# Performance work log

Hardware: AMD Instinct MI355X
Metric: run time of the kernel (lower is better)

The kernel has to match this reference:

```python
import jax, jax.numpy as jnp
import numpy as np

N, D, E, H, K = 16384, 1024, 16, 4096, 2


def setup_inputs() -> dict:
    key = jax.random.key(0)
    ks = jax.random.split(key, 6)
    s = 0.02
    return {
        "x": jax.random.normal(ks[0], (N, D), jnp.float32),
        "Wr": jax.random.normal(ks[1], (D, E), jnp.float32) * s,
        "br": jnp.zeros((E,), jnp.float32),
        "Wn": jax.random.normal(ks[2], (D, E), jnp.float32) * s,
        "bn": jnp.zeros((E,), jnp.float32),
        "W1": jax.random.normal(ks[3], (E, D, H), jnp.float32) * s,
        "b1": jnp.zeros((E, H), jnp.float32),
        "W2": jax.random.normal(ks[4], (E, H, 1), jnp.float32) * s,
        "b2": jnp.zeros((E, 1), jnp.float32),
        "k": K,
    }


def reference(x, Wr, br, Wn, bn, W1, b1, W2, b2, k):
    # Router. NOTE: faithful to source — top-k and scattered values come from
    # noise_logits; logits/noise feed only noisy_logits which is dead (only used
    # as a shape template for the -inf tensor), so the randn noise is omitted.
    noise_logits = x @ Wn + bn                      # [N, E]
    vals, idx = jax.lax.top_k(noise_logits, k)      # [N, k]
    # softmax over sparse(-inf filled) logits == softmax over top-k values,
    # scattered back; non-selected experts get exactly 0.
    probs = jax.nn.softmax(vals, axis=-1)           # [N, k]
    n = x.shape[0]
    gates = jnp.zeros((n, noise_logits.shape[-1]), x.dtype)
    gates = gates.at[jnp.arange(n)[:, None], idx].set(probs)  # [N, E]

    # Dense loop over ALL experts (as in source), masked-weighted sum.
    def step(acc, per_expert):
        w1, bb1, w2, bb2, g = per_expert
        h = jax.nn.relu(x @ w1 + bb1)               # [N, H]
        out = h @ w2 + bb2                          # [N, 1]
        return acc + out * g[:, None], None

    init = jnp.zeros((n, 1), x.dtype)
    final_out, _ = jax.lax.scan(step, init, (W1, b1, W2, b2, gates.T))
    return final_out
```

## Files before the change

kernel.cpp:

```cpp
#include <hip/hip_runtime.h>
#include <stdint.h>

#define N_TOK 16384
#define DIM   1024
#define NEXP  16
#define HID   4096

typedef unsigned short ushort_t;
typedef __bf16 bf16x8 __attribute__((ext_vector_type(8)));
typedef float  f32x4  __attribute__((ext_vector_type(4)));
typedef ushort_t u16x8 __attribute__((ext_vector_type(8)));

__device__ __forceinline__ ushort_t f2bf(float f) {
    union { float f; unsigned int u; } v; v.f = f;
    unsigned int r = v.u + 0x7fffu + ((v.u >> 16) & 1u);
    return (ushort_t)(r >> 16);
}

__device__ __forceinline__ void gl_lds16(const void* g, void* l) {
    __builtin_amdgcn_global_load_lds(
        (const __attribute__((address_space(1))) void*)g,
        (__attribute__((address_space(3))) void*)l, 16, 0, 0);
}

#define TS 72
__global__ void __launch_bounds__(256) transpose_w1_kernel(const float* __restrict__ W1,
                                                           ushort_t* __restrict__ w1t) {
    __shared__ ushort_t tileT[64 * TS];
    const int e  = blockIdx.z;
    const int h0 = blockIdx.x * 64;
    const int d0 = blockIdx.y * 64;
    const int t  = threadIdx.x;
    const int hs = t & 15;
    const int dg = t >> 4;
    const float* src = W1 + (size_t)e * DIM * HID;
    float4 rows[4];
#pragma unroll
    for (int i = 0; i < 4; ++i)
        rows[i] = *(const float4*)(src + (size_t)(d0 + dg * 4 + i) * HID + h0 + hs * 4);
#pragma unroll
    for (int j = 0; j < 4; ++j) {
        float v0 = (&rows[0].x)[j], v1 = (&rows[1].x)[j];
        float v2 = (&rows[2].x)[j], v3 = (&rows[3].x)[j];
        ushort4 col; col.x = f2bf(v0); col.y = f2bf(v1); col.z = f2bf(v2); col.w = f2bf(v3);
        *(ushort4*)&tileT[(hs * 4 + j) * TS + dg * 4] = col;
    }
    __syncthreads();
    ushort_t* dst = w1t + (size_t)e * HID * DIM;
#pragma unroll
    for (int p = 0; p < 2; ++p) {
        int r = p * 32 + (t >> 3);
        int c = t & 7;
        u16x8 fr = *(const u16x8*)&tileT[r * TS + c * 8];
        *(u16x8*)(dst + (size_t)(h0 + r) * DIM + d0 + c * 8) = fr;
    }
}

__global__ void __launch_bounds__(256) router_logits_kernel(
    const float* __restrict__ x, const float* __restrict__ Wn,
    const float* __restrict__ bn, const float* __restrict__ b2,
    ushort_t* __restrict__ xbf, int2* __restrict__ eidx,
    float2* __restrict__ probs, float* __restrict__ out) {
    int wave  = threadIdx.x >> 6;
    int lane  = threadIdx.x & 63;
    int token = blockIdx.x * 4 + wave;
    const float* xr = x + (size_t)token * DIM;
    float acc[NEXP];
#pragma unroll
    for (int e = 0; e < NEXP; ++e) acc[e] = 0.f;
    ushort_t xl[16];
#pragma unroll
    for (int i = 0; i < 16; ++i) {
        int d = lane + i * 64;
        float xv = xr[d];
        xl[i] = f2bf(xv);
        const float4* wr = (const float4*)(Wn + d * NEXP);
        float4 w0 = wr[0], w1 = wr[1], w2 = wr[2], w3 = wr[3];
        acc[0]  += xv * w0.x; acc[1]  += xv * w0.y; acc[2]  += xv * w0.z; acc[3]  += xv * w0.w;
        acc[4]  += xv * w1.x; acc[5]  += xv * w1.y; acc[6]  += xv * w1.z; acc[7]  += xv * w1.w;
        acc[8]  += xv * w2.x; acc[9]  += xv * w2.y; acc[10] += xv * w2.z; acc[11] += xv * w2.w;
        acc[12] += xv * w3.x; acc[13] += xv * w3.y; acc[14] += xv * w3.z; acc[15] += xv * w3.w;
    }
    ushort_t* xbr = xbf + (size_t)token * DIM;
#pragma unroll
    for (int i = 0; i < 16; ++i) xbr[lane + i * 64] = xl[i];
#pragma unroll
    for (int e = 0; e < NEXP; ++e) {
        float v = acc[e];
#pragma unroll
        for (int off = 32; off > 0; off >>= 1) v += __shfl_xor(v, off, 64);
        acc[e] = v + bn[e];
    }
    if (lane == 0) {
        float m0 = -1e30f; int i0 = 0;
        for (int e = 0; e < NEXP; ++e) if (acc[e] > m0) { m0 = acc[e]; i0 = e; }
        float m1 = -1e30f; int i1 = 0;
        for (int e = 0; e < NEXP; ++e) if (e != i0 && acc[e] > m1) { m1 = acc[e]; i1 = e; }
        float tq = expf(m1 - m0);
        float p0 = 1.f / (1.f + tq);
        float p1 = 1.f - p0;
        eidx[token]  = make_int2(i0, i1);
        probs[token] = make_float2(p0, p1);
        out[token]   = p0 * b2[i0] + p1 * b2[i1];
    }
}

#define NCHUNK 64
#define CHUNK  (N_TOK / NCHUNK)

__global__ void __launch_bounds__(256) hist_kernel(const int2* __restrict__ eidx,
                                                   int* __restrict__ counts) {
    __shared__ int h[NEXP];
    const int t = threadIdx.x;
    if (t < NEXP) h[t] = 0;
    __syncthreads();
    int token = blockIdx.x * CHUNK + t;
    int2 ei = eidx[token];
    atomicAdd(&h[ei.x], 1);
    atomicAdd(&h[ei.y], 1);
    __syncthreads();
    if (t < NEXP) counts[t * NCHUNK + blockIdx.x] = h[t];
}

__global__ void __launch_bounds__(1024) scan_kernel(const int* __restrict__ counts,
                                                    int* __restrict__ offs,
                                                    int* __restrict__ cnt) {
    const int w    = threadIdx.x >> 6;
    const int lane = threadIdx.x & 63;
    int v = counts[w * NCHUNK + lane];
    int orig = v;
#pragma unroll
    for (int off = 1; off < 64; off <<= 1) {
        int up = __shfl_up(v, off, 64);
        if (lane >= off) v += up;
    }
    offs[w * NCHUNK + lane] = v - orig;
    if (lane == 63) cnt[w] = v;
}

__global__ void __launch_bounds__(256) scatter_kernel(
    const int2* __restrict__ eidx, const float2* __restrict__ probs,
    const int* __restrict__ offs, int* __restrict__ tok, float* __restrict__ gate) {
    __shared__ int wcnt[4][NEXP];
    const int t = threadIdx.x;
    const int wv = t >> 6, lane = t & 63;
    const int token = blockIdx.x * CHUNK + t;
    int2  ei = eidx[token];
    float2 pr = probs[token];
    unsigned long long lmask = (1ull << lane) - 1ull;
#pragma unroll
    for (int e = 0; e < NEXP; ++e) {
        bool s = (ei.x == e) | (ei.y == e);
        unsigned long long m = __ballot(s);
        if (lane == 0) wcnt[wv][e] = __popcll(m);
    }
    __syncthreads();
#pragma unroll
    for (int e = 0; e < NEXP; ++e) {
        bool s0 = (ei.x == e);
        bool s  = s0 | (ei.y == e);
        unsigned long long m = __ballot(s);
        int base = offs[e * NCHUNK + blockIdx.x];
        for (int w = 0; w < wv; ++w) base += wcnt[w][e];
        int pos = base + __popcll(m & lmask);
        if (s) {
            tok[e * N_TOK + pos]  = token;
            gate[e * N_TOK + pos] = s0 ? pr.x : pr.y;
        }
    }
}

__global__ void __launch_bounds__(256, 2) moe_ffn_kernel(
    const ushort_t* __restrict__ xbf, const ushort_t* __restrict__ w1t,
    const float* __restrict__ b1, const float* __restrict__ w2,
    const int* __restrict__ tok, const float* __restrict__ gate,
    const int* __restrict__ cnt, float* __restrict__ out) {
    __shared__ ushort_t Alds[128 * 64];
    __shared__ ushort_t Blds[128 * 64];
    const int e  = blockIdx.z;
    const int ce = cnt[e];
    const int m0 = blockIdx.y * 128;
    if (m0 >= ce) return;
    const int h0 = blockIdx.x * 128;
    const int t    = threadIdx.x;
    const int wv   = t >> 6;
    const int lane = t & 63;
    const int quad = lane >> 4;
    const int ln   = lane & 15;
    const int wm   = (wv >> 1) * 64;
    const int wn   = (wv & 1) * 64;

    int tkid[4];
#pragma unroll
    for (int i = 0; i < 4; ++i) {
        int f = i * 256 + t;
        int r = f >> 3;
        int rr = (m0 + r < ce) ? (m0 + r) : m0;
        tkid[i] = tok[e * N_TOK + rr];
    }

    f32x4 acc[4][4];
    const f32x4 zero = {0.f, 0.f, 0.f, 0.f};
#pragma unroll
    for (int mi = 0; mi < 4; ++mi)
#pragma unroll
        for (int ni = 0; ni < 4; ++ni) acc[mi][ni] = zero;

    for (int k0 = 0; k0 < DIM; k0 += 64) {
#pragma unroll
        for (int i = 0; i < 4; ++i) {
            int f = i * 256 + t;
            int r = f >> 3, c = f & 7;
            int cs = (c ^ (r & 7)) << 3;
            const ushort_t* ga = xbf + (size_t)tkid[i] * DIM + k0 + cs;
            gl_lds16(ga, &Alds[f * 8]);
            const ushort_t* gb = w1t + ((size_t)e * HID + h0 + r) * DIM + k0 + cs;
            gl_lds16(gb, &Blds[f * 8]);
        }
        __syncthreads();
#pragma unroll
        for (int ks = 0; ks < 2; ++ks) {
            int q = ks * 4 + quad;
            int csw = (q ^ (ln & 7)) << 3;
            bf16x8 af[4], bfr[4];
#pragma unroll
            for (int mi = 0; mi < 4; ++mi)
                af[mi] = *(const bf16x8*)&Alds[(wm + mi * 16 + ln) * 64 + csw];
#pragma unroll
            for (int ni = 0; ni < 4; ++ni)
                bfr[ni] = *(const bf16x8*)&Blds[(wn + ni * 16 + ln) * 64 + csw];
#pragma unroll
            for (int mi = 0; mi < 4; ++mi)
#pragma unroll
                for (int ni = 0; ni < 4; ++ni)
                    acc[mi][ni] = __builtin_amdgcn_mfma_f32_16x16x32_bf16(
                        af[mi], bfr[ni], acc[mi][ni], 0, 0, 0);
        }
        __syncthreads();
    }

#pragma unroll
    for (int mi = 0; mi < 4; ++mi) {
        float part[4] = {0.f, 0.f, 0.f, 0.f};
#pragma unroll
        for (int ni = 0; ni < 4; ++ni) {
            int h = h0 + wn + ni * 16 + ln;
            float bb = b1[e * HID + h];
            float ww = w2[e * HID + h];
#pragma unroll
            for (int rg = 0; rg < 4; ++rg) {
                float v = acc[mi][ni][rg] + bb;
                v = v > 0.f ? v : 0.f;
                part[rg] += v * ww;
            }
        }
#pragma unroll
        for (int rg = 0; rg < 4; ++rg) {
            float v = part[rg];
            v += __shfl_xor(v, 1, 64);
            v += __shfl_xor(v, 2, 64);
            v += __shfl_xor(v, 4, 64);
            v += __shfl_xor(v, 8, 64);
            part[rg] = v;
        }
        if (ln == 0) {
#pragma unroll
            for (int rg = 0; rg < 4; ++rg) {
                int r = m0 + wm + mi * 16 + quad * 4 + rg;
                if (r < ce) {
                    int tk  = tok[e * N_TOK + r];
                    float g = gate[e * N_TOK + r];
                    atomicAdd(&out[tk], g * part[rg]);
                }
            }
        }
    }
}

extern "C" void kernel_launch(void* const* d_in, const int* in_sizes, int n_in,
                              void* d_out, int out_size, void* d_ws, size_t ws_size,
                              hipStream_t stream) {
    (void)in_sizes; (void)n_in; (void)out_size; (void)ws_size;
    const float* x  = (const float*)d_in[0];
    const float* Wn = (const float*)d_in[3];
    const float* bn = (const float*)d_in[4];
    const float* W1 = (const float*)d_in[5];
    const float* b1 = (const float*)d_in[6];
    const float* W2 = (const float*)d_in[7];
    const float* b2 = (const float*)d_in[8];
    float* out = (float*)d_out;

    char* ws = (char*)d_ws;
    ushort_t* xbf = (ushort_t*)ws;
    ushort_t* w1t = (ushort_t*)(ws + (size_t)32 * 1024 * 1024);
    char* p2 = ws + (size_t)160 * 1024 * 1024;
    size_t off = 0;
    int*    tok    = (int*)(p2 + off);    off += (size_t)NEXP * N_TOK * 4;
    float*  gate   = (float*)(p2 + off);  off += (size_t)NEXP * N_TOK * 4;
    int*    cnt    = (int*)(p2 + off);    off += 256;
    int2*   eidx   = (int2*)(p2 + off);   off += (size_t)N_TOK * 8;
    float2* probs  = (float2*)(p2 + off); off += (size_t)N_TOK * 8;
    int*    counts = (int*)(p2 + off);    off += NEXP * NCHUNK * 4;
    int*    offs   = (int*)(p2 + off);    off += NEXP * NCHUNK * 4;

    router_logits_kernel<<<N_TOK / 4, 256, 0, stream>>>(x, Wn, bn, b2, xbf, eidx, probs, out);
    hist_kernel<<<NCHUNK, 256, 0, stream>>>(eidx, counts);
    scan_kernel<<<1, 1024, 0, stream>>>(counts, offs, cnt);
    scatter_kernel<<<NCHUNK, 256, 0, stream>>>(eidx, probs, offs, tok, gate);
    transpose_w1_kernel<<<dim3(HID / 64, DIM / 64, NEXP), 256, 0, stream>>>(W1, w1t);
    moe_ffn_kernel<<<dim3(HID / 128, 64, NEXP), 256, 0, stream>>>(xbf, w1t, b1, W2, tok,
                                                                  gate, cnt, out);
}
```

Before: 831.1 us.

## Double-buffer 256x256 MoE GEMM tiles with phased LDS prefetch and merge prep kernels

```diff
diff --git a/kernel.cpp b/kernel.cpp
--- a/kernel.cpp
+++ b/kernel.cpp
@@ -24,84 +24,85 @@
 }
 
 #define TS 72
-__global__ void __launch_bounds__(256) transpose_w1_kernel(const float* __restrict__ W1,
-                                                           ushort_t* __restrict__ w1t) {
-    __shared__ ushort_t tileT[64 * TS];
-    const int e  = blockIdx.z;
-    const int h0 = blockIdx.x * 64;
-    const int d0 = blockIdx.y * 64;
-    const int t  = threadIdx.x;
-    const int hs = t & 15;
-    const int dg = t >> 4;
-    const float* src = W1 + (size_t)e * DIM * HID;
-    float4 rows[4];
-#pragma unroll
-    for (int i = 0; i < 4; ++i)
-        rows[i] = *(const float4*)(src + (size_t)(d0 + dg * 4 + i) * HID + h0 + hs * 4);
-#pragma unroll
-    for (int j = 0; j < 4; ++j) {
-        float v0 = (&rows[0].x)[j], v1 = (&rows[1].x)[j];
-        float v2 = (&rows[2].x)[j], v3 = (&rows[3].x)[j];
-        ushort4 col; col.x = f2bf(v0); col.y = f2bf(v1); col.z = f2bf(v2); col.w = f2bf(v3);
-        *(ushort4*)&tileT[(hs * 4 + j) * TS + dg * 4] = col;
-    }
-    __syncthreads();
-    ushort_t* dst = w1t + (size_t)e * HID * DIM;
-#pragma unroll
-    for (int p = 0; p < 2; ++p) {
-        int r = p * 32 + (t >> 3);
-        int c = t & 7;
-        u16x8 fr = *(const u16x8*)&tileT[r * TS + c * 8];
-        *(u16x8*)(dst + (size_t)(h0 + r) * DIM + d0 + c * 8) = fr;
-    }
-}
-
-__global__ void __launch_bounds__(256) router_logits_kernel(
+__global__ void __launch_bounds__(256) prep_kernel(
     const float* __restrict__ x, const float* __restrict__ Wn,
     const float* __restrict__ bn, const float* __restrict__ b2,
-    ushort_t* __restrict__ xbf, int2* __restrict__ eidx,
-    float2* __restrict__ probs, float* __restrict__ out) {
-    int wave  = threadIdx.x >> 6;
-    int lane  = threadIdx.x & 63;
-    int token = blockIdx.x * 4 + wave;
-    const float* xr = x + (size_t)token * DIM;
-    float acc[NEXP];
-#pragma unroll
-    for (int e = 0; e < NEXP; ++e) acc[e] = 0.f;
-    ushort_t xl[16];
-#pragma unroll
-    for (int i = 0; i < 16; ++i) {
-        int d = lane + i * 64;
-        float xv = xr[d];
-        xl[i] = f2bf(xv);
-        const float4* wr = (const float4*)(Wn + d * NEXP);
-        float4 w0 = wr[0], w1 = wr[1], w2 = wr[2], w3 = wr[3];
-        acc[0]  += xv * w0.x; acc[1]  += xv * w0.y; acc[2]  += xv * w0.z; acc[3]  += xv * w0.w;
-        acc[4]  += xv * w1.x; acc[5]  += xv * w1.y; acc[6]  += xv * w1.z; acc[7]  += xv * w1.w;
-        acc[8]  += xv * w2.x; acc[9]  += xv * w2.y; acc[10] += xv * w2.z; acc[11] += xv * w2.w;
-        acc[12] += xv * w3.x; acc[13] += xv * w3.y; acc[14] += xv * w3.z; acc[15] += xv * w3.w;
-    }
-    ushort_t* xbr = xbf + (size_t)token * DIM;
-#pragma unroll
-    for (int i = 0; i < 16; ++i) xbr[lane + i * 64] = xl[i];
-#pragma unroll
-    for (int e = 0; e < NEXP; ++e) {
-        float v = acc[e];
-#pragma unroll
-        for (int off = 32; off > 0; off >>= 1) v += __shfl_xor(v, off, 64);
-        acc[e] = v + bn[e];
-    }
-    if (lane == 0) {
-        float m0 = -1e30f; int i0 = 0;
-        for (int e = 0; e < NEXP; ++e) if (acc[e] > m0) { m0 = acc[e]; i0 = e; }
-        float m1 = -1e30f; int i1 = 0;
-        for (int e = 0; e < NEXP; ++e) if (e != i0 && acc[e] > m1) { m1 = acc[e]; i1 = e; }
-        float tq = expf(m1 - m0);
-        float p0 = 1.f / (1.f + tq);
-        float p1 = 1.f - p0;
-        eidx[token]  = make_int2(i0, i1);
-        probs[token] = make_float2(p0, p1);
-        out[token]   = p0 * b2[i0] + p1 * b2[i1];
+    const float* __restrict__ W1,
+    ushort_t* __restrict__ xbf, ushort_t* __restrict__ w1t,
+    int2* __restrict__ eidx, float2* __restrict__ probs, float* __restrict__ out) {
+    __shared__ ushort_t tileT[64 * TS];
+    if (blockIdx.z < NEXP) {
+        const int e  = blockIdx.z;
+        const int h0 = blockIdx.x * 64;
+        const int d0 = blockIdx.y * 64;
+        const int t  = threadIdx.x;
+        const int hs = t & 15;
+        const int dg = t >> 4;
+        const float* src = W1 + (size_t)e * DIM * HID;
+        float4 rows[4];
+#pragma unroll
+        for (int i = 0; i < 4; ++i)
+            rows[i] = *(const float4*)(src + (size_t)(d0 + dg * 4 + i) * HID + h0 + hs * 4);
+#pragma unroll
+        for (int j = 0; j < 4; ++j) {
+            float v0 = (&rows[0].x)[j], v1 = (&rows[1].x)[j];
+            float v2 = (&rows[2].x)[j], v3 = (&rows[3].x)[j];
+            ushort4 col; col.x = f2bf(v0); col.y = f2bf(v1); col.z = f2bf(v2); col.w = f2bf(v3);
+            *(ushort4*)&tileT[(hs * 4 + j) * TS + dg * 4] = col;
+        }
+        __syncthreads();
+        ushort_t* dst = w1t + (size_t)e * HID * DIM;
+#pragma unroll
+        for (int p = 0; p < 2; ++p) {
+            int r = p * 32 + (t >> 3);
+            int c = t & 7;
+            u16x8 fr = *(const u16x8*)&tileT[r * TS + c * 8];
+            *(u16x8*)(dst + (size_t)(h0 + r) * DIM + d0 + c * 8) = fr;
+        }
+    } else {
+        const int tb   = (blockIdx.z - NEXP) * 1024 + blockIdx.y * 64 + blockIdx.x;
+        const int wave = threadIdx.x >> 6;
+        const int lane = threadIdx.x & 63;
+        const int token = tb * 4 + wave;
+        const float* xr = x + (size_t)token * DIM;
+        float acc[NEXP];
+#pragma unroll
+        for (int e = 0; e < NEXP; ++e) acc[e] = 0.f;
+        ushort_t xl[16];
+#pragma unroll
+        for (int i = 0; i < 16; ++i) {
+            int d = lane + i * 64;
+            float xv = xr[d];
+            xl[i] = f2bf(xv);
+            const float4* wr = (const float4*)(Wn + d * NEXP);
+            float4 w0 = wr[0], w1 = wr[1], w2 = wr[2], w3 = wr[3];
+            acc[0]  += xv * w0.x; acc[1]  += xv * w0.y; acc[2]  += xv * w0.z; acc[3]  += xv * w0.w;
+            acc[4]  += xv * w1.x; acc[5]  += xv * w1.y; acc[6]  += xv * w1.z; acc[7]  += xv * w1.w;
+            acc[8]  += xv * w2.x; acc[9]  += xv * w2.y; acc[10] += xv * w2.z; acc[11] += xv * w2.w;
+            acc[12] += xv * w3.x; acc[13] += xv * w3.y; acc[14] += xv * w3.z; acc[15] += xv * w3.w;
+        }
+        ushort_t* xbr = xbf + (size_t)token * DIM;
+#pragma unroll
+        for (int i = 0; i < 16; ++i) xbr[lane + i * 64] = xl[i];
+#pragma unroll
+        for (int e = 0; e < NEXP; ++e) {
+            float v = acc[e];
+#pragma unroll
+            for (int off = 32; off > 0; off >>= 1) v += __shfl_xor(v, off, 64);
+            acc[e] = v + bn[e];
+        }
+        if (lane == 0) {
+            float m0 = -1e30f; int i0 = 0;
+            for (int e = 0; e < NEXP; ++e) if (acc[e] > m0) { m0 = acc[e]; i0 = e; }
+            float m1 = -1e30f; int i1 = 0;
+            for (int e = 0; e < NEXP; ++e) if (e != i0 && acc[e] > m1) { m1 = acc[e]; i1 = e; }
+            float tq = expf(m1 - m0);
+            float p0 = 1.f / (1.f + tq);
+            float p1 = 1.f - p0;
+            eidx[token]  = make_int2(i0, i1);
+            probs[token] = make_float2(p0, p1);
+            out[token]   = p0 * b2[i0] + p1 * b2[i1];
+        }
     }
 }
 
@@ -170,86 +171,165 @@
     }
 }
 
-__global__ void __launch_bounds__(256, 2) moe_ffn_kernel(
+__global__ void __launch_bounds__(512, 2) moe_ffn_kernel(
     const ushort_t* __restrict__ xbf, const ushort_t* __restrict__ w1t,
     const float* __restrict__ b1, const float* __restrict__ w2,
     const int* __restrict__ tok, const float* __restrict__ gate,
     const int* __restrict__ cnt, float* __restrict__ out) {
-    __shared__ ushort_t Alds[128 * 64];
-    __shared__ ushort_t Blds[128 * 64];
+    __shared__ __attribute__((aligned(16))) ushort_t Alds[2][256 * 64];
+    __shared__ __attribute__((aligned(16))) ushort_t Blds[2][256 * 64];
     const int e  = blockIdx.z;
     const int ce = cnt[e];
-    const int m0 = blockIdx.y * 128;
+    const int m0 = blockIdx.y * 256;
     if (m0 >= ce) return;
-    const int h0 = blockIdx.x * 128;
+    const int h0 = blockIdx.x * 256;
     const int t    = threadIdx.x;
     const int wv   = t >> 6;
     const int lane = t & 63;
+    const int wr   = wv >> 2;
+    const int wc   = wv & 3;
     const int quad = lane >> 4;
     const int ln   = lane & 15;
-    const int wm   = (wv >> 1) * 64;
-    const int wn   = (wv & 1) * 64;
-
-    int tkid[4];
-#pragma unroll
-    for (int i = 0; i < 4; ++i) {
-        int f = i * 256 + t;
-        int r = f >> 3;
-        int rr = (m0 + r < ce) ? (m0 + r) : m0;
-        tkid[i] = tok[e * N_TOK + rr];
-    }
-
-    f32x4 acc[4][4];
-    const f32x4 zero = {0.f, 0.f, 0.f, 0.f};
-#pragma unroll
-    for (int mi = 0; mi < 4; ++mi)
-#pragma unroll
-        for (int ni = 0; ni < 4; ++ni) acc[mi][ni] = zero;
-
-    for (int k0 = 0; k0 < DIM; k0 += 64) {
-#pragma unroll
-        for (int i = 0; i < 4; ++i) {
-            int f = i * 256 + t;
-            int r = f >> 3, c = f & 7;
-            int cs = (c ^ (r & 7)) << 3;
-            const ushort_t* ga = xbf + (size_t)tkid[i] * DIM + k0 + cs;
-            gl_lds16(ga, &Alds[f * 8]);
-            const ushort_t* gb = w1t + ((size_t)e * HID + h0 + r) * DIM + k0 + cs;
-            gl_lds16(gb, &Blds[f * 8]);
-        }
-        __syncthreads();
-#pragma unroll
-        for (int ks = 0; ks < 2; ++ks) {
-            int q = ks * 4 + quad;
-            int csw = (q ^ (ln & 7)) << 3;
-            bf16x8 af[4], bfr[4];
-#pragma unroll
-            for (int mi = 0; mi < 4; ++mi)
-                af[mi] = *(const bf16x8*)&Alds[(wm + mi * 16 + ln) * 64 + csw];
-#pragma unroll
-            for (int ni = 0; ni < 4; ++ni)
-                bfr[ni] = *(const bf16x8*)&Blds[(wn + ni * 16 + ln) * 64 + csw];
-#pragma unroll
-            for (int mi = 0; mi < 4; ++mi)
-#pragma unroll
-                for (int ni = 0; ni < 4; ++ni)
-                    acc[mi][ni] = __builtin_amdgcn_mfma_f32_16x16x32_bf16(
-                        af[mi], bfr[ni], acc[mi][ni], 0, 0, 0);
-        }
-        __syncthreads();
-    }
-
-#pragma unroll
-    for (int mi = 0; mi < 4; ++mi) {
+    const int lr   = lane >> 3;
+    const int lc   = lane & 7;
+    const int csrc = (lc ^ lr) << 3;
+
+    const int tbase = e * N_TOK;
+    const int ab = wr * 128 + wc * 16 + lr;
+    const int r00 = m0 + ab,       r01 = m0 + ab + 8;
+    const int r10 = m0 + ab + 64,  r11 = m0 + ab + 72;
+    const ushort_t* pA00 = xbf + (size_t)tok[tbase + (r00 < ce ? r00 : m0)] * DIM + csrc;
+    const ushort_t* pA01 = xbf + (size_t)tok[tbase + (r01 < ce ? r01 : m0)] * DIM + csrc;
+    const ushort_t* pA10 = xbf + (size_t)tok[tbase + (r10 < ce ? r10 : m0)] * DIM + csrc;
+    const ushort_t* pA11 = xbf + (size_t)tok[tbase + (r11 < ce ? r11 : m0)] * DIM + csrc;
+    const int bb = wc * 64 + wr * 16 + lr;
+    const ushort_t* pB00 = w1t + ((size_t)e * HID + h0 + bb) * DIM + csrc;
+    const ushort_t* pB01 = pB00 + (size_t)8 * DIM;
+    const ushort_t* pB10 = pB00 + (size_t)32 * DIM;
+    const ushort_t* pB11 = pB00 + (size_t)40 * DIM;
+    const int adst = (wr * 128 + wc * 16 + lr) * 64 + lc * 8;
+    const int bdst = (wc * 64 + wr * 16 + lr) * 64 + lc * 8;
+    const int koff0 = ((quad)     ^ (ln & 7)) << 3;
+    const int koff1 = ((quad + 4) ^ (ln & 7)) << 3;
+    const int arow = (wr * 128 + ln) * 64;
+    const int brow = (wc * 64  + ln) * 64;
+
+    ushort_t* const A0 = &Alds[0][0]; ushort_t* const A1 = &Alds[1][0];
+    ushort_t* const B0 = &Blds[0][0]; ushort_t* const B1 = &Blds[1][0];
+
+    f32x4 acc[8][4];
+    const f32x4 vzero = {0.f, 0.f, 0.f, 0.f};
+#pragma unroll
+    for (int a = 0; a < 8; ++a)
+#pragma unroll
+        for (int b = 0; b < 4; ++b) acc[a][b] = vzero;
+    bf16x8 af[8], bq0[4], bq1[4];
+
+#define STAGE_A(BUF, h, j, koff) gl_lds16(pA##h##j + (koff), (BUF) + adst + (h)*4096 + (j)*512)
+#define STAGE_B(BUF, h, j, koff) gl_lds16(pB##h##j + (koff), (BUF) + bdst + (h)*2048 + (j)*512)
+
+#define LDA(BUF, mh) do { \
+    _Pragma("unroll") for (int mi = 0; mi < 4; ++mi) { \
+        af[mi*2+0] = *(const bf16x8*)&(BUF)[arow + (mh)*4096 + mi*1024 + koff0]; \
+        af[mi*2+1] = *(const bf16x8*)&(BUF)[arow + (mh)*4096 + mi*1024 + koff1]; \
+    } } while (0)
+
+#define LDB(BUF, nh, BR) do { \
+    _Pragma("unroll") for (int ni = 0; ni < 2; ++ni) { \
+        (BR)[ni*2+0] = *(const bf16x8*)&(BUF)[brow + (nh)*2048 + ni*1024 + koff0]; \
+        (BR)[ni*2+1] = *(const bf16x8*)&(BUF)[brow + (nh)*2048 + ni*1024 + koff1]; \
+    } } while (0)
+
+#define MMAQ(mh, nh, BR) do { \
+    _Pragma("unroll") for (int ks = 0; ks < 2; ++ks) \
+    _Pragma("unroll") for (int mi = 0; mi < 4; ++mi) \
+    _Pragma("unroll") for (int ni = 0; ni < 2; ++ni) \
+        acc[(mh)*4+mi][(nh)*2+ni] = __builtin_amdgcn_mfma_f32_16x16x32_bf16( \
+            af[mi*2+ks], (BR)[ni*2+ks], acc[(mh)*4+mi][(nh)*2+ni], 0, 0, 0); \
+    } while (0)
+
+#define PH_MID() \
+    __builtin_amdgcn_s_barrier(); \
+    asm volatile("s_waitcnt lgkmcnt(0)" ::: "memory"); \
+    __builtin_amdgcn_s_setprio(1)
+#define PH_END() \
+    __builtin_amdgcn_s_setprio(0); \
+    __builtin_amdgcn_s_barrier(); \
+    asm volatile("" ::: "memory")
+#define PH_ENDB() \
+    __builtin_amdgcn_s_setprio(0); \
+    asm volatile("s_waitcnt vmcnt(6)" ::: "memory"); \
+    __builtin_amdgcn_s_barrier(); \
+    asm volatile("" ::: "memory")
+
+#define GROUP(AC, BC, AN, BN_, kA1, kN) do { \
+    LDA(AC, 0); LDB(BC, 0, bq0); \
+    STAGE_A(AN, 1, 0, kA1); STAGE_A(AN, 1, 1, kA1); \
+    PH_MID(); MMAQ(0, 0, bq0); PH_END(); \
+    LDB(BC, 1, bq1); \
+    STAGE_A(AC, 0, 0, kN); STAGE_A(AC, 0, 1, kN); \
+    PH_MID(); MMAQ(0, 1, bq1); PH_END(); \
+    LDA(AC, 1); \
+    STAGE_B(BC, 0, 0, kN); STAGE_B(BC, 0, 1, kN); \
+    PH_MID(); MMAQ(1, 1, bq1); PH_END(); \
+    STAGE_B(BC, 1, 0, kN); STAGE_B(BC, 1, 1, kN); \
+    PH_MID(); MMAQ(1, 0, bq0); PH_ENDB(); \
+    } while (0)
+
+    STAGE_A(A0, 0, 0, 0);  STAGE_A(A0, 0, 1, 0);
+    STAGE_A(A0, 1, 0, 0);  STAGE_A(A0, 1, 1, 0);
+    STAGE_B(B0, 0, 0, 0);  STAGE_B(B0, 0, 1, 0);
+    STAGE_B(B0, 1, 0, 0);  STAGE_B(B0, 1, 1, 0);
+    STAGE_A(A1, 0, 0, 64); STAGE_A(A1, 0, 1, 64);
+    STAGE_B(B1, 0, 0, 64); STAGE_B(B1, 0, 1, 64);
+    STAGE_B(B1, 1, 0, 64); STAGE_B(B1, 1, 1, 64);
+    asm volatile("s_waitcnt vmcnt(6)" ::: "memory");
+    __builtin_amdgcn_s_barrier();
+    asm volatile("" ::: "memory");
+
+#pragma unroll 1
+    for (int i = 0; i < 7; ++i) {
+        GROUP(A0, B0, A1, B1, 64, 128);
+        GROUP(A1, B1, A0, B0, 128, 192);
+        pA00 += 128; pA01 += 128; pA10 += 128; pA11 += 128;
+        pB00 += 128; pB01 += 128; pB10 += 128; pB11 += 128;
+    }
+
+    LDA(A0, 0); LDB(B0, 0, bq0);
+    STAGE_A(A1, 1, 0, 64); STAGE_A(A1, 1, 1, 64);
+    PH_MID(); MMAQ(0, 0, bq0); PH_END();
+    LDB(B0, 1, bq1);
+    PH_MID(); MMAQ(0, 1, bq1); PH_END();
+    LDA(A0, 1);
+    PH_MID(); MMAQ(1, 1, bq1); PH_END();
+    PH_MID(); MMAQ(1, 0, bq0);
+    __builtin_amdgcn_s_setprio(0);
+    asm volatile("s_waitcnt vmcnt(0)" ::: "memory");
+    __builtin_amdgcn_s_barrier();
+    asm volatile("" ::: "memory");
+
+    LDA(A1, 0); LDB(B1, 0, bq0);
+    PH_MID(); MMAQ(0, 0, bq0); PH_END();
+    LDB(B1, 1, bq1);
+    PH_MID(); MMAQ(0, 1, bq1); PH_END();
+    LDA(A1, 1);
+    PH_MID(); MMAQ(1, 1, bq1); PH_END();
+    PH_MID(); MMAQ(1, 0, bq0);
+    __builtin_amdgcn_s_setprio(0);
+
+    const float* b1p = b1 + e * HID + h0 + wc * 64;
+    const float* w2p = w2 + e * HID + h0 + wc * 64;
+#pragma unroll
+    for (int a = 0; a < 8; ++a) {
         float part[4] = {0.f, 0.f, 0.f, 0.f};
 #pragma unroll
-        for (int ni = 0; ni < 4; ++ni) {
-            int h = h0 + wn + ni * 16 + ln;
-            float bb = b1[e * HID + h];
-            float ww = w2[e * HID + h];
+        for (int b = 0; b < 4; ++b) {
+            const int hh = (b >> 1) * 32 + (b & 1) * 16 + ln;
+            const float bbv = b1p[hh];
+            const float ww  = w2p[hh];
 #pragma unroll
             for (int rg = 0; rg < 4; ++rg) {
-                float v = acc[mi][ni][rg] + bb;
+                float v = acc[a][b][rg] + bbv;
                 v = v > 0.f ? v : 0.f;
                 part[rg] += v * ww;
             }
@@ -264,17 +344,25 @@
             part[rg] = v;
         }
         if (ln == 0) {
+            const int rbase = m0 + wr * 128 + (a >> 2) * 64 + (a & 3) * 16 + quad * 4;
 #pragma unroll
             for (int rg = 0; rg < 4; ++rg) {
-                int r = m0 + wm + mi * 16 + quad * 4 + rg;
+                const int r = rbase + rg;
                 if (r < ce) {
-                    int tk  = tok[e * N_TOK + r];
-                    float g = gate[e * N_TOK + r];
-                    atomicAdd(&out[tk], g * part[rg]);
+                    atomicAdd(&out[tok[tbase + r]], gate[tbase + r] * part[rg]);
                 }
             }
         }
     }
+#undef STAGE_A
+#undef STAGE_B
+#undef LDA
+#undef LDB
+#undef MMAQ
+#undef PH_MID
+#undef PH_END
+#undef PH_ENDB
+#undef GROUP
 }
 
 extern "C" void kernel_launch(void* const* d_in, const int* in_sizes, int n_in,
@@ -303,11 +391,11 @@
     int*    counts = (int*)(p2 + off);    off += NEXP * NCHUNK * 4;
     int*    offs   = (int*)(p2 + off);    off += NEXP * NCHUNK * 4;
 
-    router_logits_kernel<<<N_TOK / 4, 256, 0, stream>>>(x, Wn, bn, b2, xbf, eidx, probs, out);
+    prep_kernel<<<dim3(64, 16, 20), 256, 0, stream>>>(x, Wn, bn, b2, W1,
+                                                      xbf, w1t, eidx, probs, out);
     hist_kernel<<<NCHUNK, 256, 0, stream>>>(eidx, counts);
     scan_kernel<<<1, 1024, 0, stream>>>(counts, offs, cnt);
     scatter_kernel<<<NCHUNK, 256, 0, stream>>>(eidx, probs, offs, tok, gate);
-    transpose_w1_kernel<<<dim3(HID / 64, DIM / 64, NEXP), 256, 0, stream>>>(W1, w1t);
-    moe_ffn_kernel<<<dim3(HID / 128, 64, NEXP), 256, 0, stream>>>(xbf, w1t, b1, W2, tok,
+    moe_ffn_kernel<<<dim3(HID / 256, 32, NEXP), 512, 0, stream>>>(xbf, w1t, b1, W2, tok,
                                                                   gate, cnt, out);
 }
```

New measurement: 983.7 us. +18.4%, slower.
